# Kernel tuning notes

Hardware: AMD Instinct MI355X
Metric: run time of the kernel (lower is better)

Reference implementation:

```python
import jax, jax.numpy as jnp
import numpy as np

EPS = 1e-6
ROPE_THETA = 10000.0


def rms_norm(x, w):
    # x: [..., hd]
    var = jnp.mean(x * x, axis=-1, keepdims=True)
    return x * jax.lax.rsqrt(var + EPS) * w


def apply_rope(x):
    # x: [B, L, nH, hd], rotate-half RoPE over sequence positions
    B, L, nH, hd = x.shape
    half = hd // 2
    inv_freq = 1.0 / (ROPE_THETA ** (jnp.arange(half, dtype=jnp.float32) / half))
    pos = jnp.arange(L, dtype=jnp.float32)
    freqs = pos[:, None] * inv_freq[None, :]          # [L, half]
    cos = jnp.cos(freqs)[None, :, None, :]            # [1, L, 1, half]
    sin = jnp.sin(freqs)[None, :, None, :]
    x1, x2 = x[..., :half], x[..., half:]
    return jnp.concatenate([x1 * cos - x2 * sin, x1 * sin + x2 * cos], axis=-1)


def setup_inputs() -> dict:
    key = jax.random.key(0)
    ks = jax.random.split(key, 5)
    B, H, W, C = 2, 48, 48, 512
    nH, nKV = 8, 4
    hd = C // nH
    s = 0.02
    return {
        "x": jax.random.normal(ks[0], (B, H, W, C), jnp.float32),
        "wq": jax.random.normal(ks[1], (C, C), jnp.float32) * s,
        "wk": jax.random.normal(ks[2], (C, nKV * hd), jnp.float32) * s,
        "wv": jax.random.normal(ks[3], (C, nKV * hd), jnp.float32) * s,
        "wo": jax.random.normal(ks[4], (C, C), jnp.float32) * s,
        "q_norm_w": jnp.ones((hd,), jnp.float32),
        "k_norm_w": jnp.ones((hd,), jnp.float32),
    }


def reference(x, wq, wk, wv, wo, q_norm_w, k_norm_w):
    B, H, W, C = x.shape
    L = H * W
    nH = 8
    hd = C // nH
    nKV = wk.shape[-1] // hd

    xf = x.reshape(B, L, C)
    q = (xf @ wq).reshape(B, L, nH, hd)
    k = (xf @ wk).reshape(B, L, nKV, hd)
    v = (xf @ wv).reshape(B, L, nKV, hd)

    q = apply_rope(rms_norm(q, q_norm_w))
    k = apply_rope(rms_norm(k, k_norm_w))

    q = q.transpose(0, 2, 1, 3)                       # [B, nH, L, hd]
    k = k.transpose(0, 2, 1, 3)                       # [B, nKV, L, hd]
    v = v.transpose(0, 2, 1, 3)
    if nKV < nH:
        rep = nH // nKV
        k = jnp.repeat(k, rep, axis=1)                # repeat_interleave over heads
        v = jnp.repeat(v, rep, axis=1)

    scale = 1.0 / jnp.sqrt(jnp.array(hd, jnp.float32))
    scores = jnp.einsum("bhqd,bhkd->bhqk", q, k) * scale
    attn = jax.nn.softmax(scores, axis=-1)
    out = jnp.einsum("bhqk,bhkd->bhqd", attn, v)      # [B, nH, L, hd]
    out = out.transpose(0, 2, 1, 3).reshape(B, H, W, C)
    return out @ wo
```

## Files before the change

kernel.cpp:

```cpp
#include <hip/hip_runtime.h>
#include <cstdint>
#include <cmath>

typedef float    f32x4  __attribute__((ext_vector_type(4)));
typedef uint32_t u32x4  __attribute__((ext_vector_type(4)));
typedef uint16_t u16x8  __attribute__((ext_vector_type(8)));
typedef __bf16   bf16x8 __attribute__((ext_vector_type(8)));

#define DEVI __device__ __forceinline__

#if __has_builtin(__builtin_amdgcn_exp2f)
DEVI float fast_exp2(float x) { return __builtin_amdgcn_exp2f(x); }
#else
DEVI float fast_exp2(float x) { return exp2f(x); }
#endif

constexpr int L   = 2304;
constexpr int C   = 512;
constexpr int NH  = 8;
constexpr int NKV = 4;
constexpr int HD  = 64;
constexpr int Bn  = 2;
constexpr int M   = Bn * L;
constexpr int NQKV = C + 2 * NKV * HD;
constexpr int NSPLIT = 4;
constexpr int KTILES = 36 / NSPLIT;

DEVI uint16_t f2bf(float f) {
  union { float f; uint32_t u; } v; v.f = f;
  uint32_t u = v.u;
  return (uint16_t)((u + 0x7fffu + ((u >> 16) & 1u)) >> 16);
}
DEVI float bf2f(uint16_t h) {
  union { uint32_t u; float f; } v; v.u = ((uint32_t)h) << 16;
  return v.f;
}
DEVI uint16_t f2h(float f) {
  _Float16 h = (_Float16)f;
  return __builtin_bit_cast(uint16_t, h);
}
DEVI float h2f(uint16_t u) {
  return (float)__builtin_bit_cast(_Float16, u);
}

DEVI bool detect_fp32(const void* qw_raw) {
  return ((const uint16_t*)qw_raw)[0] == 0;
}

DEVI f32x4 mfma_bf16(u32x4 a, u32x4 b, f32x4 c) {
  return __builtin_amdgcn_mfma_f32_16x16x32_bf16(
      __builtin_bit_cast(bf16x8, a), __builtin_bit_cast(bf16x8, b), c, 0, 0, 0);
}

DEVI uint32_t cvt_pk_bf16(float a, float b) {
  uint32_t r;
  asm("v_cvt_pk_bf16_f32 %0, %1, %2" : "=v"(r) : "v"(a), "v"(b));
  return r;
}
DEVI void permlane32_swap(uint32_t& a, uint32_t& b) {
  asm("v_permlane32_swap_b32 %0, %1" : "+v"(a), "+v"(b));
}
DEVI void permlane16_swap(uint32_t& a, uint32_t& b) {
  asm("v_permlane16_swap_b32 %0, %1" : "+v"(a), "+v"(b));
}

DEVI void gld16(const void* g, void* l) {
  __builtin_amdgcn_global_load_lds((const __attribute__((address_space(1))) void*)g,
                                   (__attribute__((address_space(3))) void*)l,
                                   16, 0, 0);
}

__global__ __launch_bounds__(256) void k_prep(
    const void* __restrict__ x,
    const void* __restrict__ wq, const void* __restrict__ wk,
    const void* __restrict__ wv, const void* __restrict__ wo,
    const void* __restrict__ qw_raw,
    uint16_t* __restrict__ xb,
    uint16_t* __restrict__ wqkvT, uint16_t* __restrict__ woT) {
  const bool f32 = detect_fp32(qw_raw);
  const int bi = blockIdx.x;
  const int t = threadIdx.x;
  if (bi >= 192) {
    const int i = ((bi - 192) * 256 + t) * 8;
    if (f32) {
      const float* xf = (const float*)x;
      const f32x4 v0 = *(const f32x4*)&xf[i];
      const f32x4 v1 = *(const f32x4*)&xf[i + 4];
      u16x8 o;
#pragma unroll
      for (int j = 0; j < 4; ++j) { o[j] = f2bf(v0[j]); o[j + 4] = f2bf(v1[j]); }
      *(u16x8*)&xb[i] = o;
    } else {
      *(u16x8*)&xb[i] = *(const u16x8*)((const uint16_t*)x + i);
    }
    return;
  }
  __shared__ uint16_t tile[64][72];
  const void* src; uint16_t* dst;
  int src_ld, col0, n0, k0;
  if (bi < 128) {
    const int nt = bi & 15, kt = bi >> 4;
    n0 = nt * 64; k0 = kt * 64;
    if (n0 < 512)      { src = wq; src_ld = 512; col0 = n0; }
    else if (n0 < 768) { src = wk; src_ld = 256; col0 = n0 - 512; }
    else               { src = wv; src_ld = 256; col0 = n0 - 768; }
    dst = wqkvT + n0 * 512 + k0;
  } else {
    const int bi2 = bi - 128;
    const int nt = bi2 & 7, kt = bi2 >> 3;
    n0 = nt * 64; k0 = kt * 64;
    src = wo; src_ld = 512; col0 = n0;
    dst = woT + n0 * 512 + k0;
  }
  const int rr = t >> 2, c4 = t & 3;
  if (f32) {
    const float* s32 = (const float*)src;
    for (int cc = c4; cc < 8; cc += 4) {
      const f32x4 v0 = *(const f32x4*)&s32[(k0 + rr) * src_ld + col0 + cc * 8];
      const f32x4 v1 = *(const f32x4*)&s32[(k0 + rr) * src_ld + col0 + cc * 8 + 4];
      for (int j = 0; j < 4; ++j) {
        tile[rr][cc * 8 + j]     = f2bf(v0[j]);
        tile[rr][cc * 8 + j + 4] = f2bf(v1[j]);
      }
    }
  } else {
    const uint16_t* s16 = (const uint16_t*)src;
    for (int cc = c4; cc < 8; cc += 4) {
      const u16x8 v = *(const u16x8*)&s16[(k0 + rr) * src_ld + col0 + cc * 8];
      for (int j = 0; j < 8; ++j) tile[rr][cc * 8 + j] = v[j];
    }
  }
  __syncthreads();
  for (int cc = c4; cc < 8; cc += 4) {
    u16x8 o;
    for (int j = 0; j < 8; ++j) o[j] = tile[cc * 8 + j][rr];
    *(u16x8*)&dst[rr * 512 + cc * 8] = o;
  }
}

DEVI void gemm128_core(const uint16_t* __restrict__ A, const uint16_t* __restrict__ Bt,
                       int m0, int n0, uint16_t* As, uint16_t* Bs, f32x4 acc[4][4]) {
  const int t = threadIdx.x;
  const int lane = t & 63, wave = t >> 6;
  const int l15 = lane & 15, quad = lane >> 4;
  const int wm = wave >> 1, wn = wave & 1;
#pragma unroll
  for (int i = 0; i < 4; ++i)
#pragma unroll
    for (int j = 0; j < 4; ++j) acc[i][j] = f32x4{0.f, 0.f, 0.f, 0.f};

  for (int k0 = 0; k0 < C; k0 += 64) {
    __syncthreads();
#pragma unroll
    for (int rr = 0; rr < 4; ++rr) {
      const int slotbase = rr * 256 + wave * 64;
      const int slot = slotbase + lane;
      const int row = slot >> 3;
      const int ch = (slot & 7) ^ (row & 7);
      gld16(&A [(m0 + row) * C + k0 + ch * 8], &As[slotbase * 8]);
      gld16(&Bt[(n0 + row) * C + k0 + ch * 8], &Bs[slotbase * 8]);
    }
    __syncthreads();
#pragma unroll
    for (int ks = 0; ks < 2; ++ks) {
      const int c = ks * 4 + quad;
      u32x4 af[4], bf[4];
#pragma unroll
      for (int mt = 0; mt < 4; ++mt) {
        const int r = wm * 64 + mt * 16 + l15;
        af[mt] = *(const u32x4*)&As[r * 64 + (c ^ (r & 7)) * 8];
      }
#pragma unroll
      for (int nt = 0; nt < 4; ++nt) {
        const int r = wn * 64 + nt * 16 + l15;
        bf[nt] = *(const u32x4*)&Bs[r * 64 + (c ^ (r & 7)) * 8];
      }
#pragma unroll
      for (int mt = 0; mt < 4; ++mt)
#pragma unroll
        for (int nt = 0; nt < 4; ++nt)
          acc[mt][nt] = mfma_bf16(af[mt], bf[nt], acc[mt][nt]);
    }
  }
}

__global__ __launch_bounds__(256, 2) void k_gemm_qkv(
    const uint16_t* __restrict__ xb, const uint16_t* __restrict__ wqkvT,
    uint16_t* __restrict__ q_p, uint16_t* __restrict__ k_p, uint16_t* __restrict__ v_t,
    const void* __restrict__ qw_raw, const void* __restrict__ kw_raw) {
  __shared__ uint16_t As[128 * 64], Bs[128 * 64];
  const bool f32 = detect_fp32(qw_raw);
  const int m0 = blockIdx.x * 128, n0 = blockIdx.y * 128;
  f32x4 acc[4][4];
  gemm128_core(xb, wqkvT, m0, n0, As, Bs, acc);
  const int t = threadIdx.x, lane = t & 63, wave = t >> 6;
  const int l15 = lane & 15, quad = lane >> 4;
  const int wm = wave >> 1, wn = wave & 1;
  const int col0 = n0 + wn * 64;

  if (col0 < C + NKV * HD) {
    const bool isq = (col0 < C);
    const void* wr = isq ? qw_raw : kw_raw;
    float w4[4];
#pragma unroll
    for (int nt = 0; nt < 4; ++nt)
      w4[nt] = f32 ? ((const float*)wr)[nt * 16 + l15]
                   : bf2f(((const uint16_t*)wr)[nt * 16 + l15]);
    const float cfreq = -0.41524101186092f;
    const float f0 = fast_exp2((float)l15 * cfreq);
    const float f1 = fast_exp2((float)(16 + l15) * cfreq);
    float sF0, cF0, sF1, cF1;
    sincosf(f0, &sF0, &cF0);
    sincosf(f1, &sF1, &cF1);
    const float sc = isq ? 0.125f * 1.44269504088896f : 1.0f;
    const int head = isq ? (col0 >> 6) : ((col0 - C) >> 6);
    uint16_t* plane = isq ? q_p : k_p;
    const int nheads = isq ? NH : NKV;
#pragma unroll
    for (int mt = 0; mt < 4; ++mt) {
      const int gm = m0 + wm * 64 + mt * 16 + quad * 4;
      const int b = gm / L;
      const int l = gm - b * L;
      uint16_t* dst = plane + ((b * nheads + head) * L + l) * HD + l15;
      float s0, c0, s1, c1;
      sincosf((float)l * f0, &s0, &c0);
      sincosf((float)l * f1, &s1, &c1);
#pragma unroll
      for (int r = 0; r < 4; ++r) {
        float x0 = acc[mt][0][r], x1 = acc[mt][1][r];
        float x2 = acc[mt][2][r], x3 = acc[mt][3][r];
        float ss = x0 * x0 + x1 * x1 + x2 * x2 + x3 * x3;
        ss += __shfl_xor(ss, 1, 64); ss += __shfl_xor(ss, 2, 64);
        ss += __shfl_xor(ss, 4, 64); ss += __shfl_xor(ss, 8, 64);
        const float inv = 1.0f / sqrtf(ss * (1.0f / 64.0f) + 1e-6f);
        x0 *= inv * w4[0]; x1 *= inv * w4[1]; x2 *= inv * w4[2]; x3 *= inv * w4[3];
        dst[r * HD +  0] = f2bf((x0 * c0 - x2 * s0) * sc);
        dst[r * HD + 16] = f2bf((x1 * c1 - x3 * s1) * sc);
        dst[r * HD + 32] = f2bf((x0 * s0 + x2 * c0) * sc);
        dst[r * HD + 48] = f2bf((x1 * s1 + x3 * c1) * sc);
        const float ns0 = s0 * cF0 + c0 * sF0, nc0 = c0 * cF0 - s0 * sF0;
        const float ns1 = s1 * cF1 + c1 * sF1, nc1 = c1 * cF1 - s1 * sF1;
        s0 = ns0; c0 = nc0; s1 = ns1; c1 = nc1;
      }
    }
  } else {
    const int vh = (col0 - C - NKV * HD) >> 6;
#pragma unroll
    for (int mt = 0; mt < 4; ++mt) {
      const int gm = m0 + wm * 64 + mt * 16 + quad * 4;
      const int b = gm / L;
      const int l = gm - b * L;
#pragma unroll
      for (int nt = 0; nt < 4; ++nt) {
        uint16_t* dst = v_t + ((b * NKV + vh) * HD + nt * 16 + l15) * L + l;
#pragma unroll
        for (int r = 0; r < 4; ++r) dst[r] = f2bf(acc[mt][nt][r]);
      }
    }
  }
}

__global__ __launch_bounds__(256, 3) void k_attn(
    const uint16_t* __restrict__ q_p, const uint16_t* __restrict__ k_p,
    const uint16_t* __restrict__ v_t,
    uint16_t* __restrict__ Ohat, float* __restrict__ lpart) {
  __shared__ uint16_t Ks[2][4096], Vs[4096];
  const int t = threadIdx.x, lane = t & 63, wave = t >> 6;
  const int l15 = lane & 15, quad = lane >> 4;

  const int bid = blockIdx.x;
  const int s   = bid / 192;
  const int rem = bid - s * 192;
  const int bkvh = rem / 24;
  const int qg   = rem - bkvh * 24;
  const int b = bkvh >> 2, kvh = bkvh & 3;
  const int u = qg * 4 + wave;
  const int h_local = u / 48;
  const int qt = u - h_local * 48;
  const int bh = b * NH + kvh * 2 + h_local;
  const int q0 = qt * 48;

  const uint16_t* qbase = q_p + (bh * L + q0) * HD;
  const uint16_t* kbase = k_p + (b * NKV + kvh) * L * HD;
  const uint16_t* vbase = v_t + (b * NKV + kvh) * HD * L;
  const int kstart = s * KTILES * 64;

  u32x4 qf[3][2];
#pragma unroll
  for (int mt = 0; mt < 3; ++mt)
#pragma unroll
    for (int ks = 0; ks < 2; ++ks)
      qf[mt][ks] = *(const u32x4*)&qbase[(mt * 16 + l15) * HD + (ks * 4 + quad) * 8];

  f32x4 O[3][4];
  float lp[3];
#pragma unroll
  for (int mt = 0; mt < 3; ++mt) {
#pragma unroll
    for (int nt = 0; nt < 4; ++nt) O[mt][nt] = f32x4{0.f, 0.f, 0.f, 0.f};
    lp[mt] = 0.f;
  }

  auto stageK = [&](int key0, int buf) {
#pragma unroll
    for (int rr = 0; rr < 2; ++rr) {
      const int slotbase = rr * 256 + wave * 64;
      const int slot = slotbase + lane;
      const int row = slot >> 3, cs = slot & 7;
      const int ch = cs ^ (row & 7);
      gld16(&kbase[(key0 + row) * HD + ch * 8], &Ks[buf][slotbase * 8]);
    }
  };
  auto stageV = [&](int key0) {
#pragma unroll
    for (int rr = 0; rr < 2; ++rr) {
      const int slotbase = rr * 256 + wave * 64;
      const int slot = slotbase + lane;
      const int row = slot >> 3, cs = slot & 7;
      const int ch = cs ^ (row & 7);
      gld16(&vbase[row * L + key0 + ch * 8], &Vs[slotbase * 8]);
    }
  };

  stageK(kstart, 0);

#pragma unroll 1
  for (int kb = 0; kb < KTILES; ++kb) {
    const int cur = kb & 1;
    __syncthreads();
    stageV(kstart + kb * 64);
    if (kb + 1 < KTILES) stageK(kstart + (kb + 1) * 64, cur ^ 1);

    u32x4 pa[3][2];

#pragma unroll
    for (int ntp = 0; ntp < 2; ++ntp) {
      f32x4 S[2][3];
#pragma unroll
      for (int ntl = 0; ntl < 2; ++ntl)
#pragma unroll
        for (int mt = 0; mt < 3; ++mt) S[ntl][mt] = f32x4{0.f, 0.f, 0.f, 0.f};
#pragma unroll
      for (int ntl = 0; ntl < 2; ++ntl) {
        const int kr = (ntp * 2 + ntl) * 16 + l15;
#pragma unroll
        for (int dks = 0; dks < 2; ++dks) {
          const int ch = dks * 4 + quad;
          const u32x4 kf = *(const u32x4*)&Ks[cur][(kr * 8 + (ch ^ (kr & 7))) * 8];
          __builtin_amdgcn_s_setprio(1);
#pragma unroll
          for (int mt = 0; mt < 3; ++mt)
            S[ntl][mt] = mfma_bf16(kf, qf[mt][dks], S[ntl][mt]);
          __builtin_amdgcn_s_setprio(0);
        }
      }
      uint32_t P32[2][3][2];
#pragma unroll
      for (int ntl = 0; ntl < 2; ++ntl)
#pragma unroll
        for (int mt = 0; mt < 3; ++mt) {
          const float p0 = fast_exp2(S[ntl][mt][0]);
          const float p1 = fast_exp2(S[ntl][mt][1]);
          const float p2 = fast_exp2(S[ntl][mt][2]);
          const float p3 = fast_exp2(S[ntl][mt][3]);
          lp[mt] += (p0 + p1) + (p2 + p3);
          P32[ntl][mt][0] = cvt_pk_bf16(p0, p1);
          P32[ntl][mt][1] = cvt_pk_bf16(p2, p3);
        }
#pragma unroll
      for (int mt = 0; mt < 3; ++mt)
#pragma unroll
        for (int j2 = 0; j2 < 2; ++j2) {
          uint32_t x = P32[0][mt][j2], y = P32[1][mt][j2];
          permlane32_swap(x, y);
          permlane16_swap(x, y);
          pa[mt][ntp][j2]     = x;
          pa[mt][ntp][2 + j2] = y;
        }
    }

    __syncthreads();

#pragma unroll
    for (int pks = 0; pks < 2; ++pks) {
#pragma unroll
      for (int nt = 0; nt < 4; ++nt) {
        const int dr = nt * 16 + l15;
        const int ch = pks * 4 + quad;
        const u32x4 vf = *(const u32x4*)&Vs[(dr * 8 + (ch ^ (dr & 7))) * 8];
        __builtin_amdgcn_s_setprio(1);
#pragma unroll
        for (int mt = 0; mt < 3; ++mt)
          O[mt][nt] = mfma_bf16(pa[mt][pks], vf, O[mt][nt]);
        __builtin_amdgcn_s_setprio(0);
      }
    }
  }

  const int obase = (s * 16 + bh) * L + q0;
#pragma unroll
  for (int mt = 0; mt < 3; ++mt) {
    float lv = lp[mt];
    lv += __shfl_xor(lv, 16, 64);
    lv += __shfl_xor(lv, 32, 64);
    if (lane < 16) lpart[obase + mt * 16 + lane] = lv;
#pragma unroll
    for (int r = 0; r < 4; ++r) {
      const float rl = 1.0f / __shfl(lv, quad * 4 + r, 64);
      const int row = obase + mt * 16 + quad * 4 + r;
#pragma unroll
      for (int nt = 0; nt < 4; ++nt)
        Ohat[row * HD + nt * 16 + l15] = f2h(O[mt][nt][r] * rl);
    }
  }
}

__global__ __launch_bounds__(256) void k_combine(
    const uint16_t* __restrict__ Ohat, const float* __restrict__ lpart,
    uint16_t* __restrict__ attn) {
  const int idx8 = blockIdx.x * 256 + threadIdx.x;
  const int row = idx8 >> 3, d0 = (idx8 & 7) * 8;
  float o[8] = {0.f, 0.f, 0.f, 0.f, 0.f, 0.f, 0.f, 0.f};
  float l = 0.f;
#pragma unroll
  for (int s = 0; s < NSPLIT; ++s) {
    const float ls = lpart[s * 16 * L + row];
    const u16x8 v = *(const u16x8*)&Ohat[(s * 16 * L + row) * HD + d0];
#pragma unroll
    for (int j = 0; j < 8; ++j) o[j] += h2f(v[j]) * ls;
    l += ls;
  }
  const int bh = row / L, lq = row - bh * L;
  const int b = bh >> 3, h = bh & 7;
  const float rl = 1.0f / l;
  u16x8 ov;
#pragma unroll
  for (int j = 0; j < 8; ++j) ov[j] = f2bf(o[j] * rl);
  *(u16x8*)&attn[(b * L + lq) * C + h * HD + d0] = ov;
}

__global__ __launch_bounds__(256, 2) void k_gemm_out(
    const uint16_t* __restrict__ attn, const uint16_t* __restrict__ woT,
    void* __restrict__ out, const void* __restrict__ qw_raw) {
  __shared__ uint16_t As[128 * 64], Bs[128 * 64];
  const bool f32 = detect_fp32(qw_raw);
  const int m0 = blockIdx.x * 128, n0 = blockIdx.y * 128;
  f32x4 acc[4][4];
  gemm128_core(attn, woT, m0, n0, As, Bs, acc);
  const int t = threadIdx.x, lane = t & 63, wave = t >> 6;
  const int l15 = lane & 15, quad = lane >> 4;
  const int wm = wave >> 1, wn = wave & 1;
#pragma unroll
  for (int mt = 0; mt < 4; ++mt) {
    const int gm = m0 + wm * 64 + mt * 16 + quad * 4;
#pragma unroll
    for (int nt = 0; nt < 4; ++nt) {
      const int gn = n0 + wn * 64 + nt * 16 + l15;
      if (f32) {
        float* o32 = (float*)out;
#pragma unroll
        for (int r = 0; r < 4; ++r) o32[(gm + r) * C + gn] = acc[mt][nt][r];
      } else {
        uint16_t* o16 = (uint16_t*)out;
#pragma unroll
        for (int r = 0; r < 4; ++r) o16[(gm + r) * C + gn] = f2bf(acc[mt][nt][r]);
      }
    }
  }
}

extern "C" void kernel_launch(void* const* d_in, const int* in_sizes, int n_in,
                              void* d_out, int out_size, void* d_ws, size_t ws_size,
                              hipStream_t stream) {
  const void* x  = d_in[0];
  const void* wq = d_in[1];
  const void* wk = d_in[2];
  const void* wv = d_in[3];
  const void* wo = d_in[4];
  const void* qw = d_in[5];
  const void* kw = d_in[6];

  uint16_t* ws = (uint16_t*)d_ws;
  uint16_t* xb    = ws;
  uint16_t* wqkvT = xb    + M * C;
  uint16_t* woT   = wqkvT + 1024 * 512;
  uint16_t* q_p   = woT   + 512 * 512;
  uint16_t* k_p   = q_p + Bn * NH  * L * HD;
  uint16_t* v_t   = k_p + Bn * NKV * L * HD;
  uint16_t* attn  = v_t + Bn * NKV * L * HD;
  uint16_t* Ohat  = attn + M * C;
  float*    lpart = (float*)(Ohat + NSPLIT * 16 * L * HD);

  k_prep      <<<dim3(192 + M * C / (256 * 8)), dim3(256), 0, stream>>>(
                  x, wq, wk, wv, wo, qw, xb, wqkvT, woT);
  k_gemm_qkv  <<<dim3(M / 128, NQKV / 128), dim3(256), 0, stream>>>(
                  xb, wqkvT, q_p, k_p, v_t, qw, kw);
  k_attn      <<<dim3(768), dim3(256), 0, stream>>>(q_p, k_p, v_t, Ohat, lpart);
  k_combine   <<<dim3(16 * L * HD / (256 * 8)), dim3(256), 0, stream>>>(Ohat, lpart, attn);
  k_gemm_out  <<<dim3(M / 128, C / 128), dim3(256), 0, stream>>>(attn, woT, d_out, qw);
}
```

Baseline: 134.5 us.

## Fuse split-KV combine into output projection GEMM A-tile load

Removes the separate combine kernel and the bf16 attn intermediate buffer. The output GEMM now reads the four partial Ohat tiles and their lse weights directly, merges them in registers, and writes the merged bf16 rows into the swizzled A tile in shared memory. This saves one launch and a full write/read of the intermediate. In exchange, each of the four column blocks repeats the combine work and reads 4x more A data, and the A load is no longer async.

```diff
diff --git a/kernel.cpp b/kernel.cpp
--- a/kernel.cpp
+++ b/kernel.cpp
@@ -383,10 +383,10 @@
 
 #pragma unroll
     for (int pks = 0; pks < 2; ++pks) {
+      const int ch = pks * 4 + quad;
 #pragma unroll
       for (int nt = 0; nt < 4; ++nt) {
         const int dr = nt * 16 + l15;
-        const int ch = pks * 4 + quad;
         const u32x4 vf = *(const u32x4*)&Vs[(dr * 8 + (ch ^ (dr & 7))) * 8];
         __builtin_amdgcn_s_setprio(1);
 #pragma unroll
@@ -415,55 +415,105 @@
   }
 }
 
-__global__ __launch_bounds__(256) void k_combine(
+__global__ __launch_bounds__(256, 2) void k_gemm_out(
     const uint16_t* __restrict__ Ohat, const float* __restrict__ lpart,
-    uint16_t* __restrict__ attn) {
-  const int idx8 = blockIdx.x * 256 + threadIdx.x;
-  const int row = idx8 >> 3, d0 = (idx8 & 7) * 8;
-  float o[8] = {0.f, 0.f, 0.f, 0.f, 0.f, 0.f, 0.f, 0.f};
-  float l = 0.f;
-#pragma unroll
-  for (int s = 0; s < NSPLIT; ++s) {
-    const float ls = lpart[s * 16 * L + row];
-    const u16x8 v = *(const u16x8*)&Ohat[(s * 16 * L + row) * HD + d0];
-#pragma unroll
-    for (int j = 0; j < 8; ++j) o[j] += h2f(v[j]) * ls;
-    l += ls;
-  }
-  const int bh = row / L, lq = row - bh * L;
-  const int b = bh >> 3, h = bh & 7;
-  const float rl = 1.0f / l;
-  u16x8 ov;
-#pragma unroll
-  for (int j = 0; j < 8; ++j) ov[j] = f2bf(o[j] * rl);
-  *(u16x8*)&attn[(b * L + lq) * C + h * HD + d0] = ov;
-}
-
-__global__ __launch_bounds__(256, 2) void k_gemm_out(
-    const uint16_t* __restrict__ attn, const uint16_t* __restrict__ woT,
+    const uint16_t* __restrict__ woT,
     void* __restrict__ out, const void* __restrict__ qw_raw) {
   __shared__ uint16_t As[128 * 64], Bs[128 * 64];
   const bool f32 = detect_fp32(qw_raw);
   const int m0 = blockIdx.x * 128, n0 = blockIdx.y * 128;
-  f32x4 acc[4][4];
-  gemm128_core(attn, woT, m0, n0, As, Bs, acc);
   const int t = threadIdx.x, lane = t & 63, wave = t >> 6;
   const int l15 = lane & 15, quad = lane >> 4;
   const int wm = wave >> 1, wn = wave & 1;
+  f32x4 acc[4][4];
+#pragma unroll
+  for (int i = 0; i < 4; ++i)
+#pragma unroll
+    for (int j = 0; j < 4; ++j) acc[i][j] = f32x4{0.f, 0.f, 0.f, 0.f};
+
+  const int r0 = t >> 1;
+  const int half = t & 1;
+  const int gm = m0 + r0;
+  const int ab = gm / L;
+  const int lq = gm - ab * L;
+
+  for (int k0 = 0; k0 < C; k0 += 64) {
+    const int h = k0 >> 6;
+    const int orow = (ab * NH + h) * L + lq;
+    const float ls0 = lpart[orow];
+    const float ls1 = lpart[16 * L + orow];
+    const float ls2 = lpart[32 * L + orow];
+    const float ls3 = lpart[48 * L + orow];
+    u16x8 oh0[4], oh1[4], oh2[4], oh3[4];
+#pragma unroll
+    for (int jj = 0; jj < 4; ++jj) {
+      const int off = half * 32 + jj * 8;
+      oh0[jj] = *(const u16x8*)&Ohat[(0 * 16 * L + orow) * HD + off];
+      oh1[jj] = *(const u16x8*)&Ohat[(1 * 16 * L + orow) * HD + off];
+      oh2[jj] = *(const u16x8*)&Ohat[(2 * 16 * L + orow) * HD + off];
+      oh3[jj] = *(const u16x8*)&Ohat[(3 * 16 * L + orow) * HD + off];
+    }
+    const float rl = 1.0f / (ls0 + ls1 + ls2 + ls3);
+    __syncthreads();
+#pragma unroll
+    for (int rr = 0; rr < 4; ++rr) {
+      const int slotbase = rr * 256 + wave * 64;
+      const int slot = slotbase + lane;
+      const int row = slot >> 3, cs = slot & 7;
+      const int ch = cs ^ (row & 7);
+      gld16(&woT[(n0 + row) * C + k0 + ch * 8], &Bs[slotbase * 8]);
+    }
+#pragma unroll
+    for (int jj = 0; jj < 4; ++jj) {
+      u16x8 ov;
+#pragma unroll
+      for (int j = 0; j < 8; ++j) {
+        float o = h2f(oh0[jj][j]) * ls0;
+        o += h2f(oh1[jj][j]) * ls1;
+        o += h2f(oh2[jj][j]) * ls2;
+        o += h2f(oh3[jj][j]) * ls3;
+        ov[j] = f2bf(o * rl);
+      }
+      const int cc = half * 4 + jj;
+      *(u16x8*)&As[r0 * 64 + (cc ^ (r0 & 7)) * 8] = ov;
+    }
+    __syncthreads();
+#pragma unroll
+    for (int ks = 0; ks < 2; ++ks) {
+      const int c = ks * 4 + quad;
+      u32x4 af[4], bf[4];
+#pragma unroll
+      for (int mt = 0; mt < 4; ++mt) {
+        const int r = wm * 64 + mt * 16 + l15;
+        af[mt] = *(const u32x4*)&As[r * 64 + (c ^ (r & 7)) * 8];
+      }
+#pragma unroll
+      for (int nt = 0; nt < 4; ++nt) {
+        const int r = wn * 64 + nt * 16 + l15;
+        bf[nt] = *(const u32x4*)&Bs[r * 64 + (c ^ (r & 7)) * 8];
+      }
+#pragma unroll
+      for (int mt = 0; mt < 4; ++mt)
+#pragma unroll
+        for (int nt = 0; nt < 4; ++nt)
+          acc[mt][nt] = mfma_bf16(af[mt], bf[nt], acc[mt][nt]);
+    }
+  }
+
 #pragma unroll
   for (int mt = 0; mt < 4; ++mt) {
-    const int gm = m0 + wm * 64 + mt * 16 + quad * 4;
+    const int ogm = m0 + wm * 64 + mt * 16 + quad * 4;
 #pragma unroll
     for (int nt = 0; nt < 4; ++nt) {
       const int gn = n0 + wn * 64 + nt * 16 + l15;
       if (f32) {
         float* o32 = (float*)out;
 #pragma unroll
-        for (int r = 0; r < 4; ++r) o32[(gm + r) * C + gn] = acc[mt][nt][r];
+        for (int r = 0; r < 4; ++r) o32[(ogm + r) * C + gn] = acc[mt][nt][r];
       } else {
         uint16_t* o16 = (uint16_t*)out;
 #pragma unroll
-        for (int r = 0; r < 4; ++r) o16[(gm + r) * C + gn] = f2bf(acc[mt][nt][r]);
+        for (int r = 0; r < 4; ++r) o16[(ogm + r) * C + gn] = f2bf(acc[mt][nt][r]);
       }
     }
   }
@@ -487,8 +537,7 @@
   uint16_t* q_p   = woT   + 512 * 512;
   uint16_t* k_p   = q_p + Bn * NH  * L * HD;
   uint16_t* v_t   = k_p + Bn * NKV * L * HD;
-  uint16_t* attn  = v_t + Bn * NKV * L * HD;
-  uint16_t* Ohat  = attn + M * C;
+  uint16_t* Ohat  = v_t + Bn * NKV * L * HD;
   float*    lpart = (float*)(Ohat + NSPLIT * 16 * L * HD);
 
   k_prep      <<<dim3(192 + M * C / (256 * 8)), dim3(256), 0, stream>>>(
@@ -496,6 +545,6 @@
   k_gemm_qkv  <<<dim3(M / 128, NQKV / 128), dim3(256), 0, stream>>>(
                   xb, wqkvT, q_p, k_p, v_t, qw, kw);
   k_attn      <<<dim3(768), dim3(256), 0, stream>>>(q_p, k_p, v_t, Ohat, lpart);
-  k_combine   <<<dim3(16 * L * HD / (256 * 8)), dim3(256), 0, stream>>>(Ohat, lpart, attn);
-  k_gemm_out  <<<dim3(M / 128, C / 128), dim3(256), 0, stream>>>(attn, woT, d_out, qw);
-}
+  k_gemm_out  <<<dim3(M / 128, C / 128), dim3(256), 0, stream>>>(
+                  Ohat, lpart, woT, d_out, qw);
+}
```

Result: slower. 145.7 us (+8.3%).
